# Optimization experiments

Hardware: AMD Instinct MI355X
Metric: run time of the kernel (lower is better)

## Reference

```python
import jax, jax.numpy as jnp
import numpy as np

N = 50000      # nodes
E = 800000     # edges (before self loops)
IN = 128       # in_channels
C = 64         # out_channels per head
H = 4          # heads (both layers)
NEG_SLOPE = 0.2


def setup_inputs():
    key = jax.random.key(0)
    ks = jax.random.split(key, 14)
    nrm = lambda k, sh, s: jax.random.normal(k, sh, dtype=jnp.float32) * s
    x = nrm(ks[0], (N, IN), 1.0)
    edge_index = jax.random.randint(ks[1], (2, E), 0, N, dtype=jnp.int32)
    batch = jnp.zeros((N,), dtype=jnp.int32)
    edge_attr = jax.random.uniform(ks[2], (E, 1), dtype=jnp.float32)
    # layer 1 params (PyG GATConv: lin, att_src, att_dst, lin_edge, att_edge, bias)
    W1 = nrm(ks[3], (IN, H * C), 1.0 / np.sqrt(IN))
    We1 = nrm(ks[4], (1, H * C), 1.0)
    att_s1 = nrm(ks[5], (H, C), 1.0 / np.sqrt(C))
    att_d1 = nrm(ks[6], (H, C), 1.0 / np.sqrt(C))
    att_e1 = nrm(ks[7], (H, C), 1.0 / np.sqrt(C))
    b1 = jnp.zeros((H * C,), dtype=jnp.float32)
    # layer 2 params (in = H*C = 256)
    W2 = nrm(ks[8], (H * C, H * C), 1.0 / np.sqrt(H * C))
    We2 = nrm(ks[9], (1, H * C), 1.0)
    att_s2 = nrm(ks[10], (H, C), 1.0 / np.sqrt(C))
    att_d2 = nrm(ks[11], (H, C), 1.0 / np.sqrt(C))
    att_e2 = nrm(ks[12], (H, C), 1.0 / np.sqrt(C))
    b2 = jnp.zeros((H * C,), dtype=jnp.float32)
    return dict(x=x, edge_index=edge_index, batch=batch, edge_attr=edge_attr,
                W1=W1, We1=We1, att_s1=att_s1, att_d1=att_d1, att_e1=att_e1, b1=b1,
                W2=W2, We2=We2, att_s2=att_s2, att_d2=att_d2, att_e2=att_e2, b2=b2)


def gat_layer(h_in, src, dst, e_attr, W, We, att_s, att_d, att_e, b):
    n = h_in.shape[0]
    h = (h_in @ W).reshape(n, H, C)                      # [N,H,C]
    a_src = jnp.einsum('nhc,hc->nh', h, att_s)           # [N,H]
    a_dst = jnp.einsum('nhc,hc->nh', h, att_d)
    e = (e_attr @ We).reshape(-1, H, C)                  # [E',H,C]
    a_edge = jnp.einsum('ehc,hc->eh', e, att_e)          # [E',H]
    alpha = jax.nn.leaky_relu(a_src[src] + a_dst[dst] + a_edge, NEG_SLOPE)
    # softmax over edges grouped by destination node
    amax = jax.ops.segment_max(alpha, dst, num_segments=n)
    amax = jnp.where(jnp.isfinite(amax), amax, 0.0)
    ex = jnp.exp(alpha - amax[dst])
    denom = jax.ops.segment_sum(ex, dst, num_segments=n)
    a = ex / (denom[dst] + 1e-16)                        # [E',H]
    out = jax.ops.segment_sum(a[:, :, None] * h[src], dst, num_segments=n)
    return out.reshape(n, H * C) + b


def reference(x, edge_index, batch, edge_attr,
              W1, We1, att_s1, att_d1, att_e1, b1,
              W2, We2, att_s2, att_d2, att_e2, b2):
    n = x.shape[0]
    # PyG GATConv default: add self loops, self-loop edge_attr = mean fill
    loop = jnp.arange(n, dtype=edge_index.dtype)
    src = jnp.concatenate([edge_index[0], loop])
    dst = jnp.concatenate([edge_index[1], loop])
    ea_fill = jnp.broadcast_to(edge_attr.mean(axis=0, keepdims=True), (n, edge_attr.shape[1]))
    ea = jnp.concatenate([edge_attr, ea_fill], axis=0)
    h1 = gat_layer(x, src, dst, ea, W1, We1, att_s1, att_d1, att_e1, b1)
    h2 = gat_layer(h1, src, dst, ea, W2, We2, att_s2, att_d2, att_e2, b2)
    return h2
```

## Files before the change

kernel.cpp:

```cpp
#include <hip/hip_runtime.h>

#define NEG_SLOPE 0.2f

typedef __attribute__((ext_vector_type(8))) short bf16x8;
typedef __attribute__((ext_vector_type(4))) float f32x4;

__device__ inline unsigned short f2bf(float x) {
  unsigned int u = __float_as_uint(x);
  u += 0x7fffu + ((u >> 16) & 1u);
  return (unsigned short)(u >> 16);
}

__device__ inline unsigned fkey(float x) {
  unsigned u = __float_as_uint(x);
  return (u >> 31) ? ~u : (u | 0x80000000u);
}
__device__ inline float fkey_dec(unsigned k) {
  unsigned u = (k & 0x80000000u) ? (k ^ 0x80000000u) : ~k;
  return __uint_as_float(u);
}


__global__ void hist_kernel(const int* __restrict__ ei, int* __restrict__ counts,
                            int E, int Etot) {
  int e = blockIdx.x * blockDim.x + threadIdx.x;
  if (e >= Etot) return;
  int d = (e < E) ? ei[E + e] : (e - E);
  atomicAdd(&counts[d], 1);
}

__global__ void mean_kernel(const float* __restrict__ ea, float* __restrict__ part, int E) {
  int i = blockIdx.x * blockDim.x + threadIdx.x;
  float s = 0.f;
  for (; i < E; i += gridDim.x * blockDim.x) s += ea[i];
#pragma unroll
  for (int off = 1; off < 64; off <<= 1) s += __shfl_xor(s, off, 64);
  __shared__ float ws_[4];
  if ((threadIdx.x & 63) == 0) ws_[threadIdx.x >> 6] = s;
  __syncthreads();
  if (threadIdx.x == 0) part[blockIdx.x] = ws_[0] + ws_[1] + ws_[2] + ws_[3];
}

__global__ void scan_blocksum(const int* __restrict__ counts, int* __restrict__ bsum, int Nn) {
  int base = blockIdx.x * 4096 + threadIdx.x * 16;
  int s = 0;
#pragma unroll
  for (int i = 0; i < 16; i++) { int idx = base + i; if (idx < Nn) s += counts[idx]; }
#pragma unroll
  for (int off = 1; off < 64; off <<= 1) s += __shfl_xor(s, off, 64);
  __shared__ int ws_[4];
  if ((threadIdx.x & 63) == 0) ws_[threadIdx.x >> 6] = s;
  __syncthreads();
  if (threadIdx.x == 0) bsum[blockIdx.x] = ws_[0] + ws_[1] + ws_[2] + ws_[3];
}

__global__ void scan_offsets(int* bsum, int nb, int* rowptrN,
                             const float* __restrict__ meanpart, float* meanv,
                             int E, int npart) {
  int t = threadIdx.x;
  float f = 0.f;
  for (int i = t; i < npart; i += 64) f += meanpart[i];
#pragma unroll
  for (int off = 1; off < 64; off <<= 1) f += __shfl_xor(f, off, 64);
  if (t == 0) {
    *meanv = f / (float)E;
    int acc = 0;
    for (int i = 0; i < nb; i++) { int v = bsum[i]; bsum[i] = acc; acc += v; }
    *rowptrN = acc;
  }
}

__global__ void scan_final(const int* __restrict__ counts, const int* __restrict__ bsum,
                           int* __restrict__ rowptr, int* __restrict__ cursor, int Nn) {
  int base = blockIdx.x * 4096 + threadIdx.x * 16;
  int v[16]; int s = 0;
#pragma unroll
  for (int i = 0; i < 16; i++) { int idx = base + i; v[i] = (idx < Nn) ? counts[idx] : 0; s += v[i]; }
  int lane = threadIdx.x & 63, wv = threadIdx.x >> 6;
  int incl = s;
#pragma unroll
  for (int off = 1; off < 64; off <<= 1) {
    int y = __shfl_up(incl, off, 64);
    if (lane >= off) incl += y;
  }
  __shared__ int wtot[4];
  if (lane == 63) wtot[wv] = incl;
  __syncthreads();
  int run = bsum[blockIdx.x] + incl - s;
  for (int i = 0; i < wv; i++) run += wtot[i];
  for (int i = 0; i < 16; i++) {
    int idx = base + i;
    if (idx < Nn) { rowptr[idx] = run; cursor[idx] = run; }
    run += v[i];
  }
}

__global__ void scatter_kernel(const int* __restrict__ ei, const float* __restrict__ eattr,
                               const float* __restrict__ meanv,
                               int* __restrict__ cursor, int2* __restrict__ epack,
                               int E, int Etot) {
  int e = blockIdx.x * blockDim.x + threadIdx.x;
  if (e >= Etot) return;
  int d, s; float ea;
  if (e < E) { d = ei[E + e]; s = ei[e]; ea = eattr[e]; }
  else       { d = e - E;     s = e - E; ea = meanv[0]; }
  int pos = atomicAdd(&cursor[d], 1);
  epack[pos] = make_int2(s, __float_as_int(ea));
}

__global__ void wtrans_kernel(const float* __restrict__ W1, unsigned short* __restrict__ Wt1,
                              const float* __restrict__ W2, unsigned short* __restrict__ Wt2,
                              const float* __restrict__ We1, const float* __restrict__ atte1,
                              const float* __restrict__ We2, const float* __restrict__ atte2,
                              float* __restrict__ weatt1, float* __restrict__ weatt2) {
  int b = blockIdx.x;
  if (b >= 384) {
    int i = threadIdx.x;
#pragma unroll
    for (int l = 0; l < 2; l++) {
      const float* We = l ? We2 : We1;
      const float* at = l ? atte2 : atte1;
      float* wo = l ? weatt2 : weatt1;
      float p = We[i] * at[i];
#pragma unroll
      for (int off = 1; off < 64; off <<= 1) p += __shfl_xor(p, off, 64);
      if ((i & 63) == 0) wo[i >> 6] = p;
    }
    return;
  }
  const float* W; unsigned short* Wt; int K, t;
  if (b < 128) { W = W1; Wt = Wt1; K = 128; t = b * 256 + threadIdx.x; }
  else         { W = W2; Wt = Wt2; K = 256; t = (b - 128) * 256 + threadIdx.x; }
  int n = t & 255, k = t >> 8;
  if (k >= K) return;
  Wt[(size_t)n * K + k] = f2bf(W[(size_t)k * 256 + n]);
}


template <int AF32>
__device__ inline bf16x8 load_a_row(const void* Ain, int gr, int K, int kpos, int M) {
  bf16x8 v = {};
  if (gr < M) {
    if (AF32) {
      const float* src = (const float*)Ain + (size_t)gr * K + kpos;
      float4 f0 = *(const float4*)src;
      float4 f1 = *(const float4*)(src + 4);
      v[0] = (short)f2bf(f0.x); v[1] = (short)f2bf(f0.y);
      v[2] = (short)f2bf(f0.z); v[3] = (short)f2bf(f0.w);
      v[4] = (short)f2bf(f1.x); v[5] = (short)f2bf(f1.y);
      v[6] = (short)f2bf(f1.z); v[7] = (short)f2bf(f1.w);
    } else {
      v = *(const bf16x8*)((const unsigned short*)Ain + (size_t)gr * K + kpos);
    }
  }
  return v;
}

#define CS_STRIDE 264

template <int AF32>
__global__ __launch_bounds__(256) void gemm_att(const void* __restrict__ Ain,
                                                const unsigned short* __restrict__ Wt,
                                                unsigned short* __restrict__ Hb,
                                                const float* __restrict__ atts,
                                                const float* __restrict__ attd,
                                                float* __restrict__ asrc,
                                                float* __restrict__ adst,
                                                unsigned* __restrict__ gmaxk,
                                                int M, int K) {
  __shared__ __align__(16) short smem[(64 + 256) * 64];
  short* As = smem;
  short* Bs = smem + 64 * 64;
  short* Cs = smem;
  const int tid = threadIdx.x;
  const int lane = tid & 63, wv = tid >> 6;
  const int l15 = lane & 15, l4 = lane >> 4;
  const int bm = blockIdx.x * 64;

  f32x4 acc[4][4] = {};

  for (int k0 = 0; k0 < K; k0 += 64) {
    {
      int r0 = tid >> 3, kcc = (tid & 7) * 8;
      bf16x8 va0 = load_a_row<AF32>(Ain, bm + r0, K, k0 + kcc, M);
      bf16x8 va1 = load_a_row<AF32>(Ain, bm + r0 + 32, K, k0 + kcc, M);
      *(bf16x8*)&As[(r0 * 64 + kcc) ^ ((r0 & 7) << 3)] = va0;
      *(bf16x8*)&As[((r0 + 32) * 64 + kcc) ^ ((r0 & 7) << 3)] = va1;
    }
    {
      int nb = tid >> 3, c = (tid & 7) * 8;
#pragma unroll
      for (int it = 0; it < 8; it++) {
        int n = nb + 32 * it;
        bf16x8 v = *(const bf16x8*)&Wt[(size_t)n * K + k0 + c];
        *(bf16x8*)&Bs[(n * 64 + c) ^ ((n & 7) << 3)] = v;
      }
    }
    __syncthreads();
    bf16x8 af[4][2], bfr[4][2];
#pragma unroll
    for (int rt = 0; rt < 4; rt++)
#pragma unroll
      for (int ks = 0; ks < 2; ks++) {
        int row = rt * 16 + l15;
        int kb = l4 * 8 + ks * 32;
        af[rt][ks] = *(const bf16x8*)&As[(row * 64 + kb) ^ ((row & 7) << 3)];
      }
#pragma unroll
    for (int ct = 0; ct < 4; ct++)
#pragma unroll
      for (int ks = 0; ks < 2; ks++) {
        int n = wv * 64 + ct * 16 + l15;
        int kb = l4 * 8 + ks * 32;
        bfr[ct][ks] = *(const bf16x8*)&Bs[(n * 64 + kb) ^ ((n & 7) << 3)];
      }
#pragma unroll
    for (int rt = 0; rt < 4; rt++)
#pragma unroll
      for (int ct = 0; ct < 4; ct++)
#pragma unroll
        for (int ks = 0; ks < 2; ks++)
          acc[rt][ct] = __builtin_amdgcn_mfma_f32_16x16x32_bf16(
              af[rt][ks], bfr[ct][ks], acc[rt][ct], 0, 0, 0);
    __syncthreads();
  }

  float s_att[4], d_att[4];
#pragma unroll
  for (int ct = 0; ct < 4; ct++) {
    s_att[ct] = atts[wv * 64 + ct * 16 + l15];
    d_att[ct] = attd[wv * 64 + ct * 16 + l15];
  }
  float ps[4][4] = {}, pd[4][4] = {};
#pragma unroll
  for (int rt = 0; rt < 4; rt++)
#pragma unroll
    for (int ct = 0; ct < 4; ct++)
#pragma unroll
      for (int i = 0; i < 4; i++) {
        float v = acc[rt][ct][i];
        int lrow = rt * 16 + l4 * 4 + i;
        Cs[lrow * CS_STRIDE + wv * 64 + ct * 16 + l15] = f2bf(v);
        ps[rt][i] = fmaf(v, s_att[ct], ps[rt][i]);
        pd[rt][i] = fmaf(v, d_att[ct], pd[rt][i]);
      }
  __syncthreads();

  {
    int row = tid >> 2, seg = tid & 3;
    int gr = bm + row;
    if (gr < M) {
      const short* srcr = &Cs[row * CS_STRIDE + seg * 64];
      unsigned short* dstr = &Hb[(size_t)gr * 256 + seg * 64];
#pragma unroll
      for (int k = 0; k < 8; k++)
        *(uint4*)&dstr[k * 8] = *(const uint4*)&srcr[k * 8];
    }
  }

#pragma unroll
  for (int rt = 0; rt < 4; rt++)
#pragma unroll
    for (int i = 0; i < 4; i++) {
#pragma unroll
      for (int off = 1; off < 16; off <<= 1) {
        ps[rt][i] += __shfl_xor(ps[rt][i], off, 64);
        pd[rt][i] += __shfl_xor(pd[rt][i], off, 64);
      }
    }
  float mx = ps[0][0];
#pragma unroll
  for (int rt = 0; rt < 4; rt++)
#pragma unroll
    for (int i = 0; i < 4; i++) mx = fmaxf(mx, ps[rt][i]);
  mx = fmaxf(mx, __shfl_xor(mx, 16, 64));
  mx = fmaxf(mx, __shfl_xor(mx, 32, 64));
  if (lane == 0) atomicMax(&gmaxk[wv * 32], fkey(mx));
  if (l15 == 0) {
#pragma unroll
    for (int rt = 0; rt < 4; rt++)
#pragma unroll
      for (int i = 0; i < 4; i++) {
        int gr = bm + rt * 16 + l4 * 4 + i;
        if (gr < M) {
          asrc[gr * 4 + wv] = ps[rt][i];
          adst[gr * 4 + wv] = pd[rt][i];
        }
      }
  }
}


#define AGG_PH1(CNT)                                                        \
  int src = 0; float w = 0.f;                                               \
  if (il < (CNT)) {                                                         \
    int2 e = epack[p + il];                                                 \
    float al = fmaf(__int_as_float(e.y), wa, asrc[e.x * 4 + hh] + ad);      \
    al = fmaxf(al, NEG_SLOPE * al);                                         \
    w = __expf(al - b);                                                     \
    src = e.x;                                                              \
  }                                                                         \
  ssum += w;

#define AGG_GATHER(i)                                                       \
  {                                                                         \
    int sl = (i) | hb16;                                                    \
    int si = __shfl(src, sl, 64);                                           \
    float wi = __shfl(w, sl, 64);                                           \
    uint2 hv = *(const uint2*)&Hb[(size_t)((unsigned)si * 256u + co)];      \
    acc.x = fmaf(wi, __uint_as_float(hv.x << 16), acc.x);                   \
    acc.y = fmaf(wi, __uint_as_float(hv.x & 0xffff0000u), acc.y);           \
    acc.z = fmaf(wi, __uint_as_float(hv.y << 16), acc.z);                   \
    acc.w = fmaf(wi, __uint_as_float(hv.y & 0xffff0000u), acc.w);           \
  }

template <int OUTBF>
__global__ __launch_bounds__(256) void gat_agg(const unsigned short* __restrict__ Hb,
                                               const float* __restrict__ asrc,
                                               const float* __restrict__ adst,
                                               const int* __restrict__ rowptr,
                                               const int2* __restrict__ epack,
                                               const float* __restrict__ weatt,
                                               const unsigned* __restrict__ gmaxk,
                                               const float* __restrict__ bias,
                                               unsigned short* __restrict__ outb,
                                               float* __restrict__ outf, int Nn) {
  int wid = (blockIdx.x * blockDim.x + threadIdx.x) >> 6;
  int lane = threadIdx.x & 63;
  if (wid >= Nn) return;
  int beg = rowptr[wid], end = rowptr[wid + 1];
  int hh = lane >> 4;
  int il = lane & 15;
  int hb16 = lane & 48;
  float wa = weatt[hh];
  float ad = adst[wid * 4 + hh];
  float braw = ad + fkey_dec(gmaxk[hh * 32]) + fmaxf(wa, 0.f);
  float b = fmaxf(braw, NEG_SLOPE * braw);
  unsigned co = (unsigned)lane * 4u;

  float ssum = 0.f;
  float4 acc = {0.f, 0.f, 0.f, 0.f};

  int p = beg;
  for (; p + 16 <= end; p += 16) {
    AGG_PH1(16)
#pragma unroll
    for (int i = 0; i < 16; i++) AGG_GATHER(i)
  }
  int cnt = end - p;
  if (cnt > 0) {
    AGG_PH1(cnt)
    for (int i = 0; i < cnt; i++) AGG_GATHER(i)
  }

#pragma unroll
  for (int off = 1; off < 16; off <<= 1) ssum += __shfl_xor(ssum, off, 64);

  float inv = 1.f / (ssum + 1e-16f);
  float4 b4 = *(const float4*)&bias[co];
  float4 r;
  r.x = fmaf(acc.x, inv, b4.x);
  r.y = fmaf(acc.y, inv, b4.y);
  r.z = fmaf(acc.z, inv, b4.z);
  r.w = fmaf(acc.w, inv, b4.w);
  if (OUTBF) {
    unsigned lo = (unsigned)f2bf(r.x) | ((unsigned)f2bf(r.y) << 16);
    unsigned hi = (unsigned)f2bf(r.z) | ((unsigned)f2bf(r.w) << 16);
    *(uint2*)&outb[(size_t)wid * 256 + co] = make_uint2(lo, hi);
  } else {
    *(float4*)&outf[(size_t)wid * 256 + co] = r;
  }
}


extern "C" void kernel_launch(void* const* d_in, const int* in_sizes, int n_in,
                              void* d_out, int out_size, void* d_ws, size_t ws_size,
                              hipStream_t stream) {
  (void)n_in; (void)out_size; (void)ws_size;
  const float* x     = (const float*)d_in[0];
  const int*   ei    = (const int*)d_in[1];
  const float* eattr = (const float*)d_in[3];
  const float* W1    = (const float*)d_in[4];
  const float* We1   = (const float*)d_in[5];
  const float* atts1 = (const float*)d_in[6];
  const float* attd1 = (const float*)d_in[7];
  const float* atte1 = (const float*)d_in[8];
  const float* b1    = (const float*)d_in[9];
  const float* W2    = (const float*)d_in[10];
  const float* We2   = (const float*)d_in[11];
  const float* atts2 = (const float*)d_in[12];
  const float* attd2 = (const float*)d_in[13];
  const float* atte2 = (const float*)d_in[14];
  const float* b2    = (const float*)d_in[15];
  float* out = (float*)d_out;

  const int Nn   = in_sizes[0] / 128;
  const int E    = in_sizes[1] / 2;
  const int Etot = E + Nn;

  char* p = (char*)d_ws;
  auto alloc = [&](size_t bytes) { void* r = (void*)p; p += (bytes + 255) & ~(size_t)255; return r; };
  int*      counts  = (int*)alloc((size_t)Nn * 4);
  unsigned* gmaxk1  = (unsigned*)alloc(512);
  unsigned* gmaxk2  = (unsigned*)alloc(512);
  char* zero_end = p;
  int*   rowptr  = (int*)alloc((size_t)(Nn + 1) * 4);
  int*   cursor  = (int*)alloc((size_t)Nn * 4);
  int2*  epack   = (int2*)alloc((size_t)Etot * 8);
  int*   bsum    = (int*)alloc(64 * 4);
  float* meanpart= (float*)alloc(512 * 4);
  float* meanv   = (float*)alloc(4);
  float* weatt1  = (float*)alloc(16);
  float* weatt2  = (float*)alloc(16);
  float* asrc    = (float*)alloc((size_t)Nn * 4 * 4);
  float* adst    = (float*)alloc((size_t)Nn * 4 * 4);
  unsigned short* hbuf = (unsigned short*)alloc((size_t)Nn * 256 * 2);
  unsigned short* h1b  = (unsigned short*)alloc((size_t)Nn * 256 * 2);
  unsigned short* Wt1  = (unsigned short*)alloc((size_t)256 * 128 * 2);
  unsigned short* Wt2  = (unsigned short*)alloc((size_t)256 * 256 * 2);

  const int NB = (Nn + 4095) / 4096;

  hipMemsetAsync(counts, 0, (size_t)(zero_end - (char*)counts), stream);

  hist_kernel<<<(Etot + 255) / 256, 256, 0, stream>>>(ei, counts, E, Etot);
  mean_kernel<<<512, 256, 0, stream>>>(eattr, meanpart, E);
  scan_blocksum<<<NB, 256, 0, stream>>>(counts, bsum, Nn);
  scan_offsets<<<1, 64, 0, stream>>>(bsum, NB, rowptr + Nn, meanpart, meanv, E, 512);
  scan_final<<<NB, 256, 0, stream>>>(counts, bsum, rowptr, cursor, Nn);
  scatter_kernel<<<(Etot + 255) / 256, 256, 0, stream>>>(ei, eattr, meanv, cursor, epack, E, Etot);
  wtrans_kernel<<<385, 256, 0, stream>>>(W1, Wt1, W2, Wt2, We1, atte1, We2, atte2,
                                         weatt1, weatt2);

  const int gemmBlocks = (Nn + 63) / 64;
  const int nodeBlocks = (Nn + 3) / 4;

  gemm_att<1><<<gemmBlocks, 256, 0, stream>>>(x, Wt1, hbuf, atts1, attd1,
                                              asrc, adst, gmaxk1, Nn, 128);
  gat_agg<1><<<nodeBlocks, 256, 0, stream>>>(hbuf, asrc, adst, rowptr, epack,
                                             weatt1, gmaxk1, b1, h1b, nullptr, Nn);
  gemm_att<0><<<gemmBlocks, 256, 0, stream>>>(h1b, Wt2, hbuf, atts2, attd2,
                                              asrc, adst, gmaxk2, Nn, 256);
  gat_agg<0><<<nodeBlocks, 256, 0, stream>>>(hbuf, asrc, adst, rowptr, epack,
                                             weatt2, gmaxk2, b2, nullptr, out, Nn);
}
```

Baseline: 330.3 us.

## Retile attention GEMM to 128x128 blocks with 2D grid over heads

The GEMM tile moves from 64 rows x 256 columns to 128 rows x 128 columns, with a 2D grid where blockIdx.y selects a pair of heads and the four waves form a 2x2 layout. Each block loads half of W per k-step and reuses it across twice as many rows. Shared memory per block drops, and the output is staged through LDS in two halves. Per-head maxima are combined across waves in LDS before a single atomicMax per head per block. In exchange, A rows are read twice (once per head pair) and there are extra barriers in the epilogue.

```diff
diff --git a/kernel.cpp b/kernel.cpp
--- a/kernel.cpp
+++ b/kernel.cpp
@@ -156,7 +156,7 @@
   return v;
 }
 
-#define CS_STRIDE 264
+#define CS2 136
 
 template <int AF32>
 __global__ __launch_bounds__(256) void gemm_att(const void* __restrict__ Ain,
@@ -168,32 +168,37 @@
                                                 float* __restrict__ adst,
                                                 unsigned* __restrict__ gmaxk,
                                                 int M, int K) {
-  __shared__ __align__(16) short smem[(64 + 256) * 64];
+  __shared__ __align__(16) short smem[(128 + 128) * 64];
+  __shared__ float gmx[4];
   short* As = smem;
-  short* Bs = smem + 64 * 64;
+  short* Bs = smem + 128 * 64;
   short* Cs = smem;
   const int tid = threadIdx.x;
   const int lane = tid & 63, wv = tid >> 6;
+  const int wm = wv >> 1, wn = wv & 1;
   const int l15 = lane & 15, l4 = lane >> 4;
-  const int bm = blockIdx.x * 64;
+  const int bm = blockIdx.x * 128;
+  const int bn2 = blockIdx.y * 128;
 
   f32x4 acc[4][4] = {};
 
   for (int k0 = 0; k0 < K; k0 += 64) {
     {
       int r0 = tid >> 3, kcc = (tid & 7) * 8;
-      bf16x8 va0 = load_a_row<AF32>(Ain, bm + r0, K, k0 + kcc, M);
-      bf16x8 va1 = load_a_row<AF32>(Ain, bm + r0 + 32, K, k0 + kcc, M);
-      *(bf16x8*)&As[(r0 * 64 + kcc) ^ ((r0 & 7) << 3)] = va0;
-      *(bf16x8*)&As[((r0 + 32) * 64 + kcc) ^ ((r0 & 7) << 3)] = va1;
+#pragma unroll
+      for (int rr = 0; rr < 4; rr++) {
+        int r = r0 + rr * 32;
+        bf16x8 v = load_a_row<AF32>(Ain, bm + r, K, k0 + kcc, M);
+        *(bf16x8*)&As[(r * 64 + kcc) ^ ((r & 7) << 3)] = v;
+      }
     }
     {
-      int nb = tid >> 3, c = (tid & 7) * 8;
-#pragma unroll
-      for (int it = 0; it < 8; it++) {
-        int n = nb + 32 * it;
-        bf16x8 v = *(const bf16x8*)&Wt[(size_t)n * K + k0 + c];
-        *(bf16x8*)&Bs[(n * 64 + c) ^ ((n & 7) << 3)] = v;
+      int n0 = tid >> 3, c = (tid & 7) * 8;
+#pragma unroll
+      for (int it = 0; it < 4; it++) {
+        int nloc = n0 + 32 * it;
+        bf16x8 v = *(const bf16x8*)&Wt[(size_t)(bn2 + nloc) * K + k0 + c];
+        *(bf16x8*)&Bs[(nloc * 64 + c) ^ ((nloc & 7) << 3)] = v;
       }
     }
     __syncthreads();
@@ -202,7 +207,7 @@
     for (int rt = 0; rt < 4; rt++)
 #pragma unroll
       for (int ks = 0; ks < 2; ks++) {
-        int row = rt * 16 + l15;
+        int row = wm * 64 + rt * 16 + l15;
         int kb = l4 * 8 + ks * 32;
         af[rt][ks] = *(const bf16x8*)&As[(row * 64 + kb) ^ ((row & 7) << 3)];
       }
@@ -210,9 +215,9 @@
     for (int ct = 0; ct < 4; ct++)
 #pragma unroll
       for (int ks = 0; ks < 2; ks++) {
-        int n = wv * 64 + ct * 16 + l15;
+        int nloc = wn * 64 + ct * 16 + l15;
         int kb = l4 * 8 + ks * 32;
-        bfr[ct][ks] = *(const bf16x8*)&Bs[(n * 64 + kb) ^ ((n & 7) << 3)];
+        bfr[ct][ks] = *(const bf16x8*)&Bs[(nloc * 64 + kb) ^ ((nloc & 7) << 3)];
       }
 #pragma unroll
     for (int rt = 0; rt < 4; rt++)
@@ -225,11 +230,12 @@
     __syncthreads();
   }
 
+  const int head = blockIdx.y * 2 + wn;
   float s_att[4], d_att[4];
 #pragma unroll
   for (int ct = 0; ct < 4; ct++) {
-    s_att[ct] = atts[wv * 64 + ct * 16 + l15];
-    d_att[ct] = attd[wv * 64 + ct * 16 + l15];
+    s_att[ct] = atts[bn2 + wn * 64 + ct * 16 + l15];
+    d_att[ct] = attd[bn2 + wn * 64 + ct * 16 + l15];
   }
   float ps[4][4] = {}, pd[4][4] = {};
 #pragma unroll
@@ -239,25 +245,9 @@
 #pragma unroll
       for (int i = 0; i < 4; i++) {
         float v = acc[rt][ct][i];
-        int lrow = rt * 16 + l4 * 4 + i;
-        Cs[lrow * CS_STRIDE + wv * 64 + ct * 16 + l15] = f2bf(v);
         ps[rt][i] = fmaf(v, s_att[ct], ps[rt][i]);
         pd[rt][i] = fmaf(v, d_att[ct], pd[rt][i]);
       }
-  __syncthreads();
-
-  {
-    int row = tid >> 2, seg = tid & 3;
-    int gr = bm + row;
-    if (gr < M) {
-      const short* srcr = &Cs[row * CS_STRIDE + seg * 64];
-      unsigned short* dstr = &Hb[(size_t)gr * 256 + seg * 64];
-#pragma unroll
-      for (int k = 0; k < 8; k++)
-        *(uint4*)&dstr[k * 8] = *(const uint4*)&srcr[k * 8];
-    }
-  }
-
 #pragma unroll
   for (int rt = 0; rt < 4; rt++)
 #pragma unroll
@@ -275,18 +265,48 @@
     for (int i = 0; i < 4; i++) mx = fmaxf(mx, ps[rt][i]);
   mx = fmaxf(mx, __shfl_xor(mx, 16, 64));
   mx = fmaxf(mx, __shfl_xor(mx, 32, 64));
-  if (lane == 0) atomicMax(&gmaxk[wv * 32], fkey(mx));
+  if (lane == 0) gmx[wv] = mx;
   if (l15 == 0) {
 #pragma unroll
     for (int rt = 0; rt < 4; rt++)
 #pragma unroll
       for (int i = 0; i < 4; i++) {
-        int gr = bm + rt * 16 + l4 * 4 + i;
+        int gr = bm + wm * 64 + rt * 16 + l4 * 4 + i;
         if (gr < M) {
-          asrc[gr * 4 + wv] = ps[rt][i];
-          adst[gr * 4 + wv] = pd[rt][i];
+          asrc[gr * 4 + head] = ps[rt][i];
+          adst[gr * 4 + head] = pd[rt][i];
         }
       }
+  }
+
+  for (int h = 0; h < 2; h++) {
+    __syncthreads();
+    if (wm == h) {
+#pragma unroll
+      for (int rt = 0; rt < 4; rt++)
+#pragma unroll
+        for (int ct = 0; ct < 4; ct++)
+#pragma unroll
+          for (int i = 0; i < 4; i++) {
+            int lrow = rt * 16 + l4 * 4 + i;
+            Cs[lrow * CS2 + wn * 64 + ct * 16 + l15] = f2bf(acc[rt][ct][i]);
+          }
+    }
+    __syncthreads();
+    int row = tid >> 2, seg = tid & 3;
+    int gr = bm + h * 64 + row;
+    if (gr < M) {
+      const short* srcr = &Cs[row * CS2 + seg * 32];
+      unsigned short* dstr = &Hb[(size_t)gr * 256 + bn2 + seg * 32];
+#pragma unroll
+      for (int k = 0; k < 4; k++)
+        *(uint4*)&dstr[k * 8] = *(const uint4*)&srcr[k * 8];
+    }
+  }
+
+  if (wv < 2 && lane == 0) {
+    float m2 = fmaxf(gmx[wv], gmx[wv + 2]);
+    atomicMax(&gmaxk[(blockIdx.y * 2 + wv) * 32], fkey(m2));
   }
 }
 
@@ -432,15 +452,15 @@
   wtrans_kernel<<<385, 256, 0, stream>>>(W1, Wt1, W2, Wt2, We1, atte1, We2, atte2,
                                          weatt1, weatt2);
 
-  const int gemmBlocks = (Nn + 63) / 64;
+  const dim3 gemmGrid((Nn + 127) / 128, 2);
   const int nodeBlocks = (Nn + 3) / 4;
 
-  gemm_att<1><<<gemmBlocks, 256, 0, stream>>>(x, Wt1, hbuf, atts1, attd1,
-                                              asrc, adst, gmaxk1, Nn, 128);
+  gemm_att<1><<<gemmGrid, 256, 0, stream>>>(x, Wt1, hbuf, atts1, attd1,
+                                            asrc, adst, gmaxk1, Nn, 128);
   gat_agg<1><<<nodeBlocks, 256, 0, stream>>>(hbuf, asrc, adst, rowptr, epack,
                                              weatt1, gmaxk1, b1, h1b, nullptr, Nn);
-  gemm_att<0><<<gemmBlocks, 256, 0, stream>>>(h1b, Wt2, hbuf, atts2, attd2,
-                                              asrc, adst, gmaxk2, Nn, 256);
+  gemm_att<0><<<gemmGrid, 256, 0, stream>>>(h1b, Wt2, hbuf, atts2, attd2,
+                                            asrc, adst, gmaxk2, Nn, 256);
   gat_agg<0><<<nodeBlocks, 256, 0, stream>>>(hbuf, asrc, adst, rowptr, epack,
                                              weatt2, gmaxk2, b2, nullptr, out, Nn);
 }
```

Result: slower. 339.8 us (+2.9%).
